# Kernel tuning notes

Hardware: AMD Instinct MI355X
Metric: run time of the kernel (lower is better)

## Reference

```python
import jax, jax.numpy as jnp
import numpy as np

N = 512        # N_ROIs (nodes)
E = N * N      # fully connected graph, COO edges
NV = 6         # n_views (edge feature dim)
C1_IN, C1_OUT = 1, 36
C2_IN, C2_OUT = 36, 24
C3_IN, C3_OUT = 24, 5


def _nnconv(x, src, dst, edge_attr, W, b, root, bias, n_nodes):
    """PyG NNConv with aggr='mean': out_i = mean_{j->i} x_j @ Theta(e_ji) + x_i @ root + bias.
    Theta = ReLU(edge_attr @ W + b) reshaped to [E, in, out] (Sequential(Linear, ReLU) edge nn)."""
    in_ch = x.shape[1]
    out_ch = root.shape[1]
    theta = jax.nn.relu(edge_attr @ W + b).reshape(-1, in_ch, out_ch)  # [E, in, out]
    msg = jnp.einsum('ei,eio->eo', x[src], theta)                      # [E, out]
    summed = jax.ops.segment_sum(msg, dst, num_segments=n_nodes)       # [N, out]
    cnt = jax.ops.segment_sum(jnp.ones((msg.shape[0], 1), x.dtype), dst, num_segments=n_nodes)
    agg = summed / jnp.maximum(cnt, 1.0)
    return agg + x @ root + bias


def setup_inputs() -> dict:
    key = jax.random.key(0)
    ks = jax.random.split(key, 12)
    s = lambda fan_in: 1.0 / np.sqrt(fan_in)
    x = jnp.ones((N, C1_IN), jnp.float32)
    edge_attr = jax.random.uniform(ks[0], (E, NV), jnp.float32)
    edge_index = jax.random.randint(ks[1], (2, E), 0, N, dtype=jnp.int64)
    return {
        'x': x, 'edge_attr': edge_attr, 'edge_index': edge_index,
        'W1': jax.random.normal(ks[2], (NV, C1_IN * C1_OUT), jnp.float32) * s(NV),
        'b1': jnp.zeros((C1_IN * C1_OUT,), jnp.float32),
        'root1': jax.random.normal(ks[3], (C1_IN, C1_OUT), jnp.float32) * s(C1_IN),
        'bias1': jnp.zeros((C1_OUT,), jnp.float32),
        'W2': jax.random.normal(ks[4], (NV, C2_IN * C2_OUT), jnp.float32) * s(NV),
        'b2': jnp.zeros((C2_IN * C2_OUT,), jnp.float32),
        'root2': jax.random.normal(ks[5], (C2_IN, C2_OUT), jnp.float32) * s(C2_IN),
        'bias2': jnp.zeros((C2_OUT,), jnp.float32),
        'W3': jax.random.normal(ks[6], (NV, C3_IN * C3_OUT), jnp.float32) * s(NV),
        'b3': jnp.zeros((C3_IN * C3_OUT,), jnp.float32),
        'root3': jax.random.normal(ks[7], (C3_IN, C3_OUT), jnp.float32) * s(C3_IN),
        'bias3': jnp.zeros((C3_OUT,), jnp.float32),
    }


def reference(x, edge_attr, edge_index, W1, b1, root1, bias1,
              W2, b2, root2, bias2, W3, b3, root3, bias3):
    src, dst = edge_index[0], edge_index[1]
    n = x.shape[0]
    h = jax.nn.relu(_nnconv(x, src, dst, edge_attr, W1, b1, root1, bias1, n))
    h = jax.nn.relu(_nnconv(h, src, dst, edge_attr, W2, b2, root2, bias2, n))
    h = jax.nn.relu(_nnconv(h, src, dst, edge_attr, W3, b3, root3, bias3, n))
    # CBT: cbt[a, b] = sum_f |h[b, f] - h[a, f]|  (repeat/transpose/abs/sum in torch)
    cbt = jnp.sum(jnp.abs(h[None, :, :] - h[:, None, :]), axis=2)  # [N, N]
    return cbt
```

## Files before the change

kernel.cpp:

```cpp
#include <hip/hip_runtime.h>

#define N_NODES 512
#define N_EDGES (512 * 512)

typedef _Float16 f16x8 __attribute__((ext_vector_type(8)));
typedef float f32x4 __attribute__((ext_vector_type(4)));

__device__ __forceinline__ unsigned pkf16(float a, float b) {
  return __builtin_bit_cast(unsigned, __builtin_amdgcn_cvt_pkrtz(a, b));
}

__global__ void hist_k(const int* __restrict__ dst, int* __restrict__ counts) {
  __shared__ int lh[N_NODES];
  for (int i = threadIdx.x; i < N_NODES; i += blockDim.x) lh[i] = 0;
  __syncthreads();
  const int stride = gridDim.x * blockDim.x;
  for (int e = blockIdx.x * blockDim.x + threadIdx.x; e < N_EDGES; e += stride)
    atomicAdd(&lh[dst[e]], 1);
  __syncthreads();
  for (int i = threadIdx.x; i < N_NODES; i += blockDim.x) {
    int c = lh[i];
    if (c) atomicAdd(&counts[i], c);
  }
}

__global__ void scan_k(const int* __restrict__ counts, int* __restrict__ offsets,
                       int* __restrict__ cursor) {
  __shared__ int tmp[N_NODES];
  const int t = threadIdx.x;
  const int c = counts[t];
  tmp[t] = c;
  __syncthreads();
  for (int d = 1; d < N_NODES; d <<= 1) {
    int add = (t >= d) ? tmp[t - d] : 0;
    __syncthreads();
    tmp[t] += add;
    __syncthreads();
  }
  offsets[t + 1] = tmp[t];
  if (t == 0) offsets[0] = 0;
  cursor[t] = tmp[t] - c;
}

__launch_bounds__(512)
__global__ void scatter3_k(const float* __restrict__ ea, const int* __restrict__ src,
                           const int* __restrict__ dst, int* __restrict__ cursor,
                           uint4* __restrict__ eaPk, int* __restrict__ srcSorted) {
  __shared__ int lhist[N_NODES];
  __shared__ int gb[N_NODES];
  const int t = threadIdx.x;
  const int c0 = blockIdx.x * 4096;
  lhist[t] = 0;
  __syncthreads();
  int d[8], r[8];
#pragma unroll
  for (int j = 0; j < 8; j++) {
    d[j] = dst[c0 + t + j * 512];
    r[j] = atomicAdd(&lhist[d[j]], 1);
  }
  __syncthreads();
  gb[t] = atomicAdd(&cursor[t], lhist[t]);
  __syncthreads();
#pragma unroll
  for (int j = 0; j < 8; j++) {
    const int e = c0 + t + j * 512;
    const int pos = gb[d[j]] + r[j];
    const float2* er = reinterpret_cast<const float2*>(ea + (size_t)e * 6);
    const float2 a0 = er[0], a1 = er[1], a2 = er[2];
    uint4 pk;
    pk.x = pkf16(a0.x, a0.y);
    pk.y = pkf16(a1.x, a1.y);
    pk.z = pkf16(a2.x, a2.y);
    pk.w = 0x00003C00u;
    eaPk[pos] = pk;
    srcSorted[pos] = src[e];
  }
}

__global__ void packAll2_k(const float* __restrict__ W1, const float* __restrict__ b1,
                           const float* __restrict__ W2, const float* __restrict__ b2,
                           const float* __restrict__ W3, const float* __restrict__ b3,
                           uint4* __restrict__ wpk) {
  const int t = blockIdx.x * 256 + threadIdx.x;
  uint4 r = make_uint4(0u, 0u, 0x00000000u, pkf16(-1.f, 0.f));
  if (t < 48) {
    if (t < 36) {
      r.x = pkf16(W1[0 * 36 + t], W1[1 * 36 + t]);
      r.y = pkf16(W1[2 * 36 + t], W1[3 * 36 + t]);
      r.z = pkf16(W1[4 * 36 + t], W1[5 * 36 + t]);
      r.w = pkf16(b1[t], 0.f);
    }
    wpk[t] = r;
  } else if (t < 1200) {
    const int q = t - 48;
    const int tile = q >> 4, row = q & 15;
    const int i = tile >> 1, o = ((tile & 1) << 4) + row;
    if (o < 24) {
      const int p = i * 24 + o;
      r.x = pkf16(W2[0 * 864 + p], W2[1 * 864 + p]);
      r.y = pkf16(W2[2 * 864 + p], W2[3 * 864 + p]);
      r.z = pkf16(W2[4 * 864 + p], W2[5 * 864 + p]);
      r.w = pkf16(b2[p], 0.f);
    }
    wpk[t] = r;
  } else if (t < 1328) {
    const int q = t - 1200;
    const int tile = q >> 4, row = q & 15;
    if (row < 15) {
      const int i = 3 * tile + row / 5;
      const int o = row % 5;
      const int p = i * 5 + o;
      r.x = pkf16(W3[0 * 120 + p], W3[1 * 120 + p]);
      r.y = pkf16(W3[2 * 120 + p], W3[3 * 120 + p]);
      r.z = pkf16(W3[4 * 120 + p], W3[5 * 120 + p]);
      r.w = pkf16(b3[p], 0.f);
    }
    wpk[t] = r;
  }
}

__launch_bounds__(512, 4)
__global__ void conv1_k(const float* __restrict__ x,
                        const uint4* __restrict__ eaPk, const int* __restrict__ srcSorted,
                        const int* __restrict__ offsets, const uint4* __restrict__ Wpk,
                        const float* __restrict__ root, const float* __restrict__ bias,
                        float* __restrict__ hnext) {
  __shared__ float hS[N_NODES];
  __shared__ float pAcc[8][48];
  const int tid = threadIdx.x, w = tid >> 6, l = tid & 63;
  const int node = blockIdx.x;
  const int off = offsets[node], cnt = offsets[node + 1] - off;
  const int col = l & 15, crow = (l >> 4) << 2;

  if (tid < N_NODES) hS[tid] = x[tid];

  f16x8 afr[3];
  f32x4 acc[3];
#pragma unroll
  for (int t = 0; t < 3; t++) {
    uint4 wv = make_uint4(0u, 0u, 0u, 0u);
    if (l < 16) wv = Wpk[t * 16 + l];
    afr[t] = __builtin_bit_cast(f16x8, wv);
    acc[t] = (f32x4){0.f, 0.f, 0.f, 0.f};
  }
  __syncthreads();

  const int NG = (cnt + 15) >> 4;
  const f32x4 zero4 = {0.f, 0.f, 0.f, 0.f};
  for (int g = w; g < NG; g += 8) {
    const int pos = g * 16 + col;
    const bool v = pos < cnt;
    const int s = v ? srcSorted[off + pos] : 0;
    uint4 bv = make_uint4(0u, 0u, 0u, 0u);
    if (l < 16 && v) bv = eaPk[off + pos];
    const f16x8 bfr = __builtin_bit_cast(f16x8, bv);
    const float hv = hS[s];
#pragma unroll
    for (int t = 0; t < 3; t++) {
      f32x4 th = __builtin_amdgcn_mfma_f32_16x16x32_f16(afr[t], bfr, zero4, 0, 0, 0);
#pragma unroll
      for (int r = 0; r < 4; r++)
        acc[t][r] = fmaf(fmaxf(th[r], 0.f), hv, acc[t][r]);
    }
  }
#pragma unroll
  for (int t = 0; t < 3; t++)
#pragma unroll
    for (int r = 0; r < 4; r++) {
      float vv = acc[t][r];
      vv += __shfl_xor(vv, 1); vv += __shfl_xor(vv, 2);
      vv += __shfl_xor(vv, 4); vv += __shfl_xor(vv, 8);
      if (col == 0) pAcc[w][t * 16 + crow + r] = vv;
    }
  __syncthreads();
  if (tid < 36) {
    const int o = tid;
    float sagg = 0.f;
#pragma unroll
    for (int ww = 0; ww < 8; ww++) sagg += pAcc[ww][o];
    const float agg = sagg / fmaxf((float)cnt, 1.f);
    const float r2 = fmaf(hS[node], root[o], bias[o]);
    hnext[node * 36 + o] = fmaxf(agg + r2, 0.f);
  }
}

__launch_bounds__(512, 4)
__global__ void conv2_k(const float* __restrict__ hprev,
                        const uint4* __restrict__ eaPk, const int* __restrict__ srcSorted,
                        const int* __restrict__ offsets, const uint4* __restrict__ Wpk,
                        const float* __restrict__ root, const float* __restrict__ bias,
                        float* __restrict__ hnext) {
  __shared__ float hS[N_NODES * 37];
  __shared__ float pAcc[1152];
  const int tid = threadIdx.x, w = tid >> 6, l = tid & 63;
  const int node = blockIdx.x;
  const int off = offsets[node], cnt = offsets[node + 1] - off;
  const int col = l & 15, crow = (l >> 4) << 2;

  for (int n = tid; n < N_NODES * 36; n += 512) hS[n + n / 36] = hprev[n];

  f16x8 afr[5][2];
  f32x4 acc[5][2];
  int hidx[5];
#pragma unroll
  for (int jp = 0; jp < 5; jp++) {
    const int tp = w + 8 * jp;
    hidx[jp] = (tp < 36) ? tp : 0;
#pragma unroll
    for (int hh = 0; hh < 2; hh++) {
      uint4 wv = make_uint4(0u, 0u, 0u, 0u);
      if (tp < 36 && l < 16) wv = Wpk[(2 * tp + hh) * 16 + l];
      afr[jp][hh] = __builtin_bit_cast(f16x8, wv);
      acc[jp][hh] = (f32x4){0.f, 0.f, 0.f, 0.f};
    }
  }
  __syncthreads();

  const int NG = (cnt + 15) >> 4;
  const f32x4 zero4 = {0.f, 0.f, 0.f, 0.f};

  uint4 bv_c = make_uint4(0u, 0u, 0u, 0u);
  int s_c = 0;
  auto gload = [&](int g) {
    const int pos = g * 16 + col;
    const bool v = pos < cnt;
    s_c = v ? srcSorted[off + pos] : 0;
    bv_c = make_uint4(0u, 0u, 0u, 0u);
    if (l < 16 && v) bv_c = eaPk[off + pos];
  };

  if (NG > 0) gload(0);
  for (int g = 0; g < NG; g++) {
    const int sb = s_c * 37;
    float hcur[5];
#pragma unroll
    for (int jp = 0; jp < 5; jp++) hcur[jp] = hS[sb + hidx[jp]];
    const f16x8 bfr = __builtin_bit_cast(f16x8, bv_c);
    if (g + 1 < NG) gload(g + 1);
    f32x4 t0 = __builtin_amdgcn_mfma_f32_16x16x32_f16(afr[0][0], bfr, zero4, 0, 0, 0);
    f32x4 t1 = __builtin_amdgcn_mfma_f32_16x16x32_f16(afr[0][1], bfr, zero4, 0, 0, 0);
#pragma unroll
    for (int jp = 0; jp < 5; jp++) {
      f32x4 n0, n1;
      if (jp < 4) {
        n0 = __builtin_amdgcn_mfma_f32_16x16x32_f16(afr[jp + 1][0], bfr, zero4, 0, 0, 0);
        n1 = __builtin_amdgcn_mfma_f32_16x16x32_f16(afr[jp + 1][1], bfr, zero4, 0, 0, 0);
      }
      const float hv = hcur[jp];
#pragma unroll
      for (int r = 0; r < 4; r++) {
        acc[jp][0][r] = fmaf(fmaxf(t0[r], 0.f), hv, acc[jp][0][r]);
        acc[jp][1][r] = fmaf(fmaxf(t1[r], 0.f), hv, acc[jp][1][r]);
      }
      if (jp < 4) { t0 = n0; t1 = n1; }
    }
  }

#pragma unroll
  for (int jp = 0; jp < 5; jp++) {
    const int tp = w + 8 * jp;
    if (tp < 36) {
#pragma unroll
      for (int hh = 0; hh < 2; hh++)
#pragma unroll
        for (int r = 0; r < 4; r++) {
          float vv = acc[jp][hh][r];
          vv += __shfl_xor(vv, 1); vv += __shfl_xor(vv, 2);
          vv += __shfl_xor(vv, 4); vv += __shfl_xor(vv, 8);
          if (col == 0) pAcc[tp * 32 + hh * 16 + crow + r] = vv;
        }
    }
  }
  __syncthreads();
  if (tid < 24) {
    const int o = tid;
    float sagg = 0.f;
    for (int i = 0; i < 36; i++) sagg += pAcc[i * 32 + o];
    const float agg = sagg / fmaxf((float)cnt, 1.f);
    float r2 = bias[o];
    for (int i = 0; i < 36; i++) r2 = fmaf(hS[node * 37 + i], root[i * 24 + o], r2);
    hnext[node * 24 + o] = fmaxf(agg + r2, 0.f);
  }
}

__launch_bounds__(512, 4)
__global__ void conv3_k(const float* __restrict__ hprev,
                        const uint4* __restrict__ eaPk, const int* __restrict__ srcSorted,
                        const int* __restrict__ offsets, const uint4* __restrict__ Wpk,
                        const float* __restrict__ root, const float* __restrict__ bias,
                        float* __restrict__ hnext) {
  __shared__ float hS[N_NODES * 25];
  __shared__ float pAcc[8][128];
  const int tid = threadIdx.x, w = tid >> 6, l = tid & 63;
  const int node = blockIdx.x;
  const int off = offsets[node], cnt = offsets[node + 1] - off;
  const int col = l & 15, crow = (l >> 4) << 2;

  for (int n = tid; n < N_NODES * 24; n += 512) hS[n + n / 24] = hprev[n];

  f16x8 afr[8];
  f32x4 acc[8];
#pragma unroll
  for (int t = 0; t < 8; t++) {
    uint4 wv = make_uint4(0u, 0u, 0u, 0u);
    if (l < 16) wv = Wpk[t * 16 + l];
    afr[t] = __builtin_bit_cast(f16x8, wv);
    acc[t] = (f32x4){0.f, 0.f, 0.f, 0.f};
  }
  __syncthreads();

  const int NG = (cnt + 15) >> 4;
  const f32x4 zero4 = {0.f, 0.f, 0.f, 0.f};
  for (int g = w; g < NG; g += 8) {
    const int pos = g * 16 + col;
    const bool v = pos < cnt;
    const int s = v ? srcSorted[off + pos] : 0;
    uint4 bv = make_uint4(0u, 0u, 0u, 0u);
    if (l < 16 && v) bv = eaPk[off + pos];
    const f16x8 bfr = __builtin_bit_cast(f16x8, bv);
    const int sb = s * 25;
#pragma unroll
    for (int t = 0; t < 8; t++) {
      f32x4 th = __builtin_amdgcn_mfma_f32_16x16x32_f16(afr[t], bfr, zero4, 0, 0, 0);
      const float h0 = hS[sb + 3 * t];
      const float h1 = hS[sb + 3 * t + 1];
      const float h2 = hS[sb + 3 * t + 2];
#pragma unroll
      for (int r = 0; r < 4; r++) {
        const int row = crow + r;
        const float hv = (row < 5) ? h0 : ((row < 10) ? h1 : h2);
        acc[t][r] = fmaf(fmaxf(th[r], 0.f), hv, acc[t][r]);
      }
    }
  }
#pragma unroll
  for (int t = 0; t < 8; t++)
#pragma unroll
    for (int r = 0; r < 4; r++) {
      float vv = acc[t][r];
      vv += __shfl_xor(vv, 1); vv += __shfl_xor(vv, 2);
      vv += __shfl_xor(vv, 4); vv += __shfl_xor(vv, 8);
      if (col == 0) pAcc[w][t * 16 + crow + r] = vv;
    }
  __syncthreads();
  if (tid < 128) {
    float s8 = 0.f;
#pragma unroll
    for (int ww = 0; ww < 8; ww++) s8 += pAcc[ww][tid];
    pAcc[0][tid] = s8;
  }
  __syncthreads();
  if (tid < 5) {
    const int o = tid;
    float sagg = 0.f;
    for (int i = 0; i < 24; i++) {
      const int t = i / 3, iloc = i - 3 * t;
      sagg += pAcc[0][t * 16 + iloc * 5 + o];
    }
    const float agg = sagg / fmaxf((float)cnt, 1.f);
    float r2 = bias[o];
    for (int i = 0; i < 24; i++) r2 = fmaf(hS[node * 25 + i], root[i * 5 + o], r2);
    hnext[node * 5 + o] = fmaxf(agg + r2, 0.f);
  }
}

__global__ void cbt_k(const float* __restrict__ h3, float* __restrict__ out) {
  __shared__ float sh[N_NODES * 5];
  for (int i = threadIdx.x; i < N_NODES * 5; i += blockDim.x) sh[i] = h3[i];
  __syncthreads();
  const int a = blockIdx.x;
  float ha0 = sh[a * 5 + 0], ha1 = sh[a * 5 + 1], ha2 = sh[a * 5 + 2],
        ha3 = sh[a * 5 + 3], ha4 = sh[a * 5 + 4];
  for (int b = threadIdx.x; b < N_NODES; b += blockDim.x) {
    float s = fabsf(sh[b * 5 + 0] - ha0) + fabsf(sh[b * 5 + 1] - ha1) +
              fabsf(sh[b * 5 + 2] - ha2) + fabsf(sh[b * 5 + 3] - ha3) +
              fabsf(sh[b * 5 + 4] - ha4);
    out[a * N_NODES + b] = s;
  }
}

extern "C" void kernel_launch(void* const* d_in, const int* in_sizes, int n_in,
                              void* d_out, int out_size, void* d_ws, size_t ws_size,
                              hipStream_t stream) {
  const float* x     = (const float*)d_in[0];
  const float* ea    = (const float*)d_in[1];
  const int*   ei    = (const int*)d_in[2];
  const float* W1    = (const float*)d_in[3];
  const float* b1    = (const float*)d_in[4];
  const float* root1 = (const float*)d_in[5];
  const float* bias1 = (const float*)d_in[6];
  const float* W2    = (const float*)d_in[7];
  const float* b2    = (const float*)d_in[8];
  const float* root2 = (const float*)d_in[9];
  const float* bias2 = (const float*)d_in[10];
  const float* W3    = (const float*)d_in[11];
  const float* b3    = (const float*)d_in[12];
  const float* root3 = (const float*)d_in[13];
  const float* bias3 = (const float*)d_in[14];

  const int* src = ei;
  const int* dst = ei + N_EDGES;

  char* ws = (char*)d_ws;
  int* counts    = (int*)(ws + 0);
  int* offsets   = (int*)(ws + 4096);
  int* cursor    = (int*)(ws + 8192);
  uint4* eaPk    = (uint4*)(ws + 16384);
  int* srcSorted = (int*)(ws + 16384 + N_EDGES * 16);
  char* p2       = ws + 16384 + N_EDGES * 20;
  float* h1      = (float*)(p2);
  float* h2_     = h1 + N_NODES * 36;
  float* h3      = h2_ + N_NODES * 24;
  uint4* wpkAll  = (uint4*)(p2 + 256 * 1024);
  uint4* wpk1    = wpkAll;
  uint4* wpk2    = wpkAll + 48;
  uint4* wpk3    = wpkAll + 1200;

  hipMemsetAsync(counts, 0, N_NODES * sizeof(int), stream);
  hist_k<<<64, 256, 0, stream>>>(dst, counts);
  scan_k<<<1, N_NODES, 0, stream>>>(counts, offsets, cursor);
  scatter3_k<<<N_EDGES / 4096, 512, 0, stream>>>(ea, src, dst, cursor, eaPk, srcSorted);
  packAll2_k<<<6, 256, 0, stream>>>(W1, b1, W2, b2, W3, b3, wpkAll);

  conv1_k<<<N_NODES, 512, 0, stream>>>(x, eaPk, srcSorted, offsets, wpk1, root1, bias1, h1);
  conv2_k<<<N_NODES, 512, 0, stream>>>(h1, eaPk, srcSorted, offsets, wpk2, root2, bias2, h2_);
  conv3_k<<<N_NODES, 512, 0, stream>>>(h2_, eaPk, srcSorted, offsets, wpk3, root3, bias3, h3);

  cbt_k<<<N_NODES, 256, 0, stream>>>(h3, (float*)d_out);
}
```

Baseline: 102.6 us.

## Pad per-node edge segments to 16 and double waves per conv block

The scan pads each destination's edge count to a multiple of 16 and the packed edge buffers are zero-filled, so the conv kernels can drop per-lane bounds checks. The conv kernels now launch 1024 threads (16 waves) per node, splitting edge groups across twice as many waves, with a two-phase partial reduction in conv2. The LDS padding of node feature rows is removed. The risks are an extra memset of the enlarged edge buffer, higher register pressure under the tighter launch bounds, and possible LDS bank conflicts.

```diff
diff --git a/kernel.cpp b/kernel.cpp
--- a/kernel.cpp
+++ b/kernel.cpp
@@ -2,6 +2,7 @@
 
 #define N_NODES 512
 #define N_EDGES (512 * 512)
+#define EP (N_EDGES + 8192)
 
 typedef _Float16 f16x8 __attribute__((ext_vector_type(8)));
 typedef float f32x4 __attribute__((ext_vector_type(4)));
@@ -24,12 +25,12 @@
   }
 }
 
-__global__ void scan_k(const int* __restrict__ counts, int* __restrict__ offsets,
+__global__ void scan_k(const int* __restrict__ counts, int* __restrict__ pOff,
                        int* __restrict__ cursor) {
   __shared__ int tmp[N_NODES];
   const int t = threadIdx.x;
-  const int c = counts[t];
-  tmp[t] = c;
+  const int pc = (counts[t] + 15) & ~15;
+  tmp[t] = pc;
   __syncthreads();
   for (int d = 1; d < N_NODES; d <<= 1) {
     int add = (t >= d) ? tmp[t - d] : 0;
@@ -37,9 +38,9 @@
     tmp[t] += add;
     __syncthreads();
   }
-  offsets[t + 1] = tmp[t];
-  if (t == 0) offsets[0] = 0;
-  cursor[t] = tmp[t] - c;
+  pOff[t + 1] = tmp[t];
+  if (t == 0) pOff[0] = 0;
+  cursor[t] = tmp[t] - pc;
 }
 
 __launch_bounds__(512)
@@ -119,17 +120,18 @@
   }
 }
 
-__launch_bounds__(512, 4)
+__launch_bounds__(1024, 4)
 __global__ void conv1_k(const float* __restrict__ x,
                         const uint4* __restrict__ eaPk, const int* __restrict__ srcSorted,
-                        const int* __restrict__ offsets, const uint4* __restrict__ Wpk,
+                        const int* __restrict__ pOff, const int* __restrict__ counts,
+                        const uint4* __restrict__ Wpk,
                         const float* __restrict__ root, const float* __restrict__ bias,
                         float* __restrict__ hnext) {
   __shared__ float hS[N_NODES];
-  __shared__ float pAcc[8][48];
+  __shared__ float pAcc[16][48];
   const int tid = threadIdx.x, w = tid >> 6, l = tid & 63;
   const int node = blockIdx.x;
-  const int off = offsets[node], cnt = offsets[node + 1] - off;
+  const int off = pOff[node], cnt = counts[node];
   const int col = l & 15, crow = (l >> 4) << 2;
 
   if (tid < N_NODES) hS[tid] = x[tid];
@@ -147,12 +149,11 @@
 
   const int NG = (cnt + 15) >> 4;
   const f32x4 zero4 = {0.f, 0.f, 0.f, 0.f};
-  for (int g = w; g < NG; g += 8) {
-    const int pos = g * 16 + col;
-    const bool v = pos < cnt;
-    const int s = v ? srcSorted[off + pos] : 0;
-    uint4 bv = make_uint4(0u, 0u, 0u, 0u);
-    if (l < 16 && v) bv = eaPk[off + pos];
+  uint4 bv = make_uint4(0u, 0u, 0u, 0u);
+  for (int g = w; g < NG; g += 16) {
+    const int pos = off + g * 16 + col;
+    const int s = srcSorted[pos];
+    if (l < 16) bv = eaPk[pos];
     const f16x8 bfr = __builtin_bit_cast(f16x8, bv);
     const float hv = hS[s];
 #pragma unroll
@@ -177,34 +178,36 @@
     const int o = tid;
     float sagg = 0.f;
 #pragma unroll
-    for (int ww = 0; ww < 8; ww++) sagg += pAcc[ww][o];
+    for (int ww = 0; ww < 16; ww++) sagg += pAcc[ww][o];
     const float agg = sagg / fmaxf((float)cnt, 1.f);
     const float r2 = fmaf(hS[node], root[o], bias[o]);
     hnext[node * 36 + o] = fmaxf(agg + r2, 0.f);
   }
 }
 
-__launch_bounds__(512, 4)
+__launch_bounds__(1024, 4)
 __global__ void conv2_k(const float* __restrict__ hprev,
                         const uint4* __restrict__ eaPk, const int* __restrict__ srcSorted,
-                        const int* __restrict__ offsets, const uint4* __restrict__ Wpk,
+                        const int* __restrict__ pOff, const int* __restrict__ counts,
+                        const uint4* __restrict__ Wpk,
                         const float* __restrict__ root, const float* __restrict__ bias,
                         float* __restrict__ hnext) {
-  __shared__ float hS[N_NODES * 37];
+  __shared__ float hS[N_NODES * 36];
   __shared__ float pAcc[1152];
   const int tid = threadIdx.x, w = tid >> 6, l = tid & 63;
+  const int w8 = w & 7, gh = w >> 3;
   const int node = blockIdx.x;
-  const int off = offsets[node], cnt = offsets[node + 1] - off;
+  const int off = pOff[node], cnt = counts[node];
   const int col = l & 15, crow = (l >> 4) << 2;
 
-  for (int n = tid; n < N_NODES * 36; n += 512) hS[n + n / 36] = hprev[n];
+  for (int n = tid; n < N_NODES * 36; n += 1024) hS[n] = hprev[n];
 
   f16x8 afr[5][2];
   f32x4 acc[5][2];
   int hidx[5];
 #pragma unroll
   for (int jp = 0; jp < 5; jp++) {
-    const int tp = w + 8 * jp;
+    const int tp = w8 + 8 * jp;
     hidx[jp] = (tp < 36) ? tp : 0;
 #pragma unroll
     for (int hh = 0; hh < 2; hh++) {
@@ -222,21 +225,19 @@
   uint4 bv_c = make_uint4(0u, 0u, 0u, 0u);
   int s_c = 0;
   auto gload = [&](int g) {
-    const int pos = g * 16 + col;
-    const bool v = pos < cnt;
-    s_c = v ? srcSorted[off + pos] : 0;
-    bv_c = make_uint4(0u, 0u, 0u, 0u);
-    if (l < 16 && v) bv_c = eaPk[off + pos];
+    const int pos = off + g * 16 + col;
+    s_c = srcSorted[pos];
+    if (l < 16) bv_c = eaPk[pos];
   };
 
-  if (NG > 0) gload(0);
-  for (int g = 0; g < NG; g++) {
-    const int sb = s_c * 37;
+  if (gh < NG) gload(gh);
+  for (int g = gh; g < NG; g += 2) {
+    const int sb = s_c * 36;
     float hcur[5];
 #pragma unroll
     for (int jp = 0; jp < 5; jp++) hcur[jp] = hS[sb + hidx[jp]];
     const f16x8 bfr = __builtin_bit_cast(f16x8, bv_c);
-    if (g + 1 < NG) gload(g + 1);
+    if (g + 2 < NG) gload(g + 2);
     f32x4 t0 = __builtin_amdgcn_mfma_f32_16x16x32_f16(afr[0][0], bfr, zero4, 0, 0, 0);
     f32x4 t1 = __builtin_amdgcn_mfma_f32_16x16x32_f16(afr[0][1], bfr, zero4, 0, 0, 0);
 #pragma unroll
@@ -256,19 +257,39 @@
     }
   }
 
-#pragma unroll
-  for (int jp = 0; jp < 5; jp++) {
-    const int tp = w + 8 * jp;
-    if (tp < 36) {
-#pragma unroll
-      for (int hh = 0; hh < 2; hh++)
-#pragma unroll
-        for (int r = 0; r < 4; r++) {
-          float vv = acc[jp][hh][r];
-          vv += __shfl_xor(vv, 1); vv += __shfl_xor(vv, 2);
-          vv += __shfl_xor(vv, 4); vv += __shfl_xor(vv, 8);
-          if (col == 0) pAcc[tp * 32 + hh * 16 + crow + r] = vv;
-        }
+  if (w < 8) {
+#pragma unroll
+    for (int jp = 0; jp < 5; jp++) {
+      const int tp = w8 + 8 * jp;
+      if (tp < 36) {
+#pragma unroll
+        for (int hh = 0; hh < 2; hh++)
+#pragma unroll
+          for (int r = 0; r < 4; r++) {
+            float vv = acc[jp][hh][r];
+            vv += __shfl_xor(vv, 1); vv += __shfl_xor(vv, 2);
+            vv += __shfl_xor(vv, 4); vv += __shfl_xor(vv, 8);
+            if (col == 0) pAcc[tp * 32 + hh * 16 + crow + r] = vv;
+          }
+      }
+    }
+  }
+  __syncthreads();
+  if (w >= 8) {
+#pragma unroll
+    for (int jp = 0; jp < 5; jp++) {
+      const int tp = w8 + 8 * jp;
+      if (tp < 36) {
+#pragma unroll
+        for (int hh = 0; hh < 2; hh++)
+#pragma unroll
+          for (int r = 0; r < 4; r++) {
+            float vv = acc[jp][hh][r];
+            vv += __shfl_xor(vv, 1); vv += __shfl_xor(vv, 2);
+            vv += __shfl_xor(vv, 4); vv += __shfl_xor(vv, 8);
+            if (col == 0) pAcc[tp * 32 + hh * 16 + crow + r] += vv;
+          }
+      }
     }
   }
   __syncthreads();
@@ -278,25 +299,26 @@
     for (int i = 0; i < 36; i++) sagg += pAcc[i * 32 + o];
     const float agg = sagg / fmaxf((float)cnt, 1.f);
     float r2 = bias[o];
-    for (int i = 0; i < 36; i++) r2 = fmaf(hS[node * 37 + i], root[i * 24 + o], r2);
+    for (int i = 0; i < 36; i++) r2 = fmaf(hS[node * 36 + i], root[i * 24 + o], r2);
     hnext[node * 24 + o] = fmaxf(agg + r2, 0.f);
   }
 }
 
-__launch_bounds__(512, 4)
+__launch_bounds__(1024, 4)
 __global__ void conv3_k(const float* __restrict__ hprev,
                         const uint4* __restrict__ eaPk, const int* __restrict__ srcSorted,
-                        const int* __restrict__ offsets, const uint4* __restrict__ Wpk,
+                        const int* __restrict__ pOff, const int* __restrict__ counts,
+                        const uint4* __restrict__ Wpk,
                         const float* __restrict__ root, const float* __restrict__ bias,
                         float* __restrict__ hnext) {
-  __shared__ float hS[N_NODES * 25];
-  __shared__ float pAcc[8][128];
+  __shared__ float hS[N_NODES * 24];
+  __shared__ float pAcc[16][128];
   const int tid = threadIdx.x, w = tid >> 6, l = tid & 63;
   const int node = blockIdx.x;
-  const int off = offsets[node], cnt = offsets[node + 1] - off;
+  const int off = pOff[node], cnt = counts[node];
   const int col = l & 15, crow = (l >> 4) << 2;
 
-  for (int n = tid; n < N_NODES * 24; n += 512) hS[n + n / 24] = hprev[n];
+  for (int n = tid; n < N_NODES * 24; n += 1024) hS[n] = hprev[n];
 
   f16x8 afr[8];
   f32x4 acc[8];
@@ -311,14 +333,13 @@
 
   const int NG = (cnt + 15) >> 4;
   const f32x4 zero4 = {0.f, 0.f, 0.f, 0.f};
-  for (int g = w; g < NG; g += 8) {
-    const int pos = g * 16 + col;
-    const bool v = pos < cnt;
-    const int s = v ? srcSorted[off + pos] : 0;
-    uint4 bv = make_uint4(0u, 0u, 0u, 0u);
-    if (l < 16 && v) bv = eaPk[off + pos];
+  uint4 bv = make_uint4(0u, 0u, 0u, 0u);
+  for (int g = w; g < NG; g += 16) {
+    const int pos = off + g * 16 + col;
+    const int s = srcSorted[pos];
+    if (l < 16) bv = eaPk[pos];
     const f16x8 bfr = __builtin_bit_cast(f16x8, bv);
-    const int sb = s * 25;
+    const int sb = s * 24;
 #pragma unroll
     for (int t = 0; t < 8; t++) {
       f32x4 th = __builtin_amdgcn_mfma_f32_16x16x32_f16(afr[t], bfr, zero4, 0, 0, 0);
@@ -346,7 +367,7 @@
   if (tid < 128) {
     float s8 = 0.f;
 #pragma unroll
-    for (int ww = 0; ww < 8; ww++) s8 += pAcc[ww][tid];
+    for (int ww = 0; ww < 16; ww++) s8 += pAcc[ww][tid];
     pAcc[0][tid] = s8;
   }
   __syncthreads();
@@ -359,7 +380,7 @@
     }
     const float agg = sagg / fmaxf((float)cnt, 1.f);
     float r2 = bias[o];
-    for (int i = 0; i < 24; i++) r2 = fmaf(hS[node * 25 + i], root[i * 5 + o], r2);
+    for (int i = 0; i < 24; i++) r2 = fmaf(hS[node * 24 + i], root[i * 5 + o], r2);
     hnext[node * 5 + o] = fmaxf(agg + r2, 0.f);
   }
 }
@@ -403,11 +424,11 @@
 
   char* ws = (char*)d_ws;
   int* counts    = (int*)(ws + 0);
-  int* offsets   = (int*)(ws + 4096);
+  int* pOff      = (int*)(ws + 4096);
   int* cursor    = (int*)(ws + 8192);
   uint4* eaPk    = (uint4*)(ws + 16384);
-  int* srcSorted = (int*)(ws + 16384 + N_EDGES * 16);
-  char* p2       = ws + 16384 + N_EDGES * 20;
+  int* srcSorted = (int*)(ws + 16384 + (size_t)EP * 16);
+  char* p2       = ws + 16384 + (size_t)EP * 20;
   float* h1      = (float*)(p2);
   float* h2_     = h1 + N_NODES * 36;
   float* h3      = h2_ + N_NODES * 24;
@@ -417,14 +438,15 @@
   uint4* wpk3    = wpkAll + 1200;
 
   hipMemsetAsync(counts, 0, N_NODES * sizeof(int), stream);
+  hipMemsetAsync(eaPk, 0, (size_t)EP * 20, stream);
   hist_k<<<64, 256, 0, stream>>>(dst, counts);
-  scan_k<<<1, N_NODES, 0, stream>>>(counts, offsets, cursor);
+  scan_k<<<1, N_NODES, 0, stream>>>(counts, pOff, cursor);
   scatter3_k<<<N_EDGES / 4096, 512, 0, stream>>>(ea, src, dst, cursor, eaPk, srcSorted);
   packAll2_k<<<6, 256, 0, stream>>>(W1, b1, W2, b2, W3, b3, wpkAll);
 
-  conv1_k<<<N_NODES, 512, 0, stream>>>(x, eaPk, srcSorted, offsets, wpk1, root1, bias1, h1);
-  conv2_k<<<N_NODES, 512, 0, stream>>>(h1, eaPk, srcSorted, offsets, wpk2, root2, bias2, h2_);
-  conv3_k<<<N_NODES, 512, 0, stream>>>(h2_, eaPk, srcSorted, offsets, wpk3, root3, bias3, h3);
+  conv1_k<<<N_NODES, 1024, 0, stream>>>(x, eaPk, srcSorted, pOff, counts, wpk1, root1, bias1, h1);
+  conv2_k<<<N_NODES, 1024, 0, stream>>>(h1, eaPk, srcSorted, pOff, counts, wpk2, root2, bias2, h2_);
+  conv3_k<<<N_NODES, 1024, 0, stream>>>(h2_, eaPk, srcSorted, pOff, counts, wpk3, root3, bias3, h3);
 
   cbt_k<<<N_NODES, 256, 0, stream>>>(h3, (float*)d_out);
 }
```

Result: slower. 127.8 us (+24.6%).
